# Kernel tuning notes

Hardware: AMD Instinct MI355X
Metric: run time of the kernel (lower is better)

Reference implementation:

```python
import jax, jax.numpy as jnp
import numpy as np

N_LEVELS = 8
N_FEATS = 2
LOG2_T = 19
BASE_RES = 16.0
FINEST_RES = 2048.0
BOX_MIN, BOX_MAX = 0.0, 1.0
B_GROWTH = float(np.exp((np.log(FINEST_RES) - np.log(BASE_RES)) / (N_LEVELS - 1)))  # = 2.0
HASH_MASK = (1 << LOG2_T) - 1
BATCH = 4194304


def setup_inputs() -> dict:
    key = jax.random.key(0)
    kx, kt = jax.random.split(key)
    x = jax.random.uniform(kx, (BATCH, 1), dtype=jnp.float32, minval=BOX_MIN, maxval=BOX_MAX)
    # n_levels separate embedding tables, init uniform in [-1e-4, 1e-4]
    tables = jax.random.uniform(kt, (N_LEVELS, 1 << LOG2_T, N_FEATS), dtype=jnp.float32,
                                minval=-1e-4, maxval=1e-4)
    return {"x": x, "tables": tables}


def reference(x, tables):
    # x: [B, 1] in [BOX_MIN, BOX_MAX]; tables: [L, 2^T, F]
    outs = []
    for i in range(N_LEVELS):
        resolution = jnp.floor(BASE_RES * (B_GROWTH ** i))
        grid_size = (BOX_MAX - BOX_MIN) / resolution
        idx = jnp.floor((x - BOX_MIN) / grid_size)            # [B, 1] cell index (float)
        interval_min = BOX_MIN + idx * grid_size              # [B, 1]
        interval_max = interval_min + grid_size               # [B, 1]
        # two interval vertices: idx and idx+1; 1-D spatial hash = index & (2^T - 1)
        verts = jnp.concatenate([idx, idx + 1.0], axis=-1).astype(jnp.int32)  # [B, 2]
        hashed = jnp.bitwise_and(verts, HASH_MASK)            # [B, 2]
        emb = tables[i][hashed]                               # [B, 2, F] gather
        w = (x - interval_min) / (interval_max - interval_min)  # [B, 1]
        c = emb[:, 0] * (1.0 - w) + emb[:, 1] * w             # [B, F]
        outs.append(c)
    return jnp.concatenate(outs, axis=-1)                     # [B, L*F]
```

## Files before the change

kernel.cpp:

```cpp
#include <hip/hip_runtime.h>


#define NGP_BATCH   4194304
#define NGP_TSIZE   (1 << 19)
#define BLOCK       512
#define PPB         4096
#define KITER       (PPB / (BLOCK/4))
#define NBODY       (KITER / 4)

typedef float f32x4 __attribute__((ext_vector_type(4)));

__global__ __launch_bounds__(BLOCK) void hashenc_kernel(
    const float* __restrict__ x,
    const float* __restrict__ tables,
    float* __restrict__ out)
{
    __shared__ float4 sm4[4080];

    const int tid = threadIdx.x;

#pragma unroll
    for (int l = 0; l < 8; ++l) {
        const int n   = 16 << l;
        const int off = 16 * ((1 << l) - 1);
        const float2* __restrict__ src =
            reinterpret_cast<const float2*>(tables) + (size_t)l * NGP_TSIZE;
        for (int e = tid; e < n; e += BLOCK) {
            const float2 a = src[e];
            const float2 b = src[e + 1];
            sm4[off + e] = make_float4(a.x, a.y, b.x - a.x, b.y - a.y);
        }
    }
    __syncthreads();

    const int q  = tid >> 2;
    const int s  = tid & 3;
    const int l0 = 2 * s;
    const int l1 = 2 * s + 1;
    const float res0 = (float)(16 << l0);
    const float res1 = (float)(16 << l1);
    const int   off0 = 16 * ((1 << l0) - 1);
    const int   off1 = 16 * ((1 << l1) - 1);

    const int P0 = blockIdx.x * PPB;
    f32x4* __restrict__ out4 = reinterpret_cast<f32x4*>(out);

    float xc[4], xn[4];
#pragma unroll
    for (int j = 0; j < 4; ++j)
        xc[j] = x[P0 + q + 128 * j];

#pragma unroll
    for (int m = 0; m < NBODY; ++m) {
        if (m + 1 < NBODY) {
#pragma unroll
            for (int j = 0; j < 4; ++j)
                xn[j] = x[P0 + q + 128 * (4 * (m + 1) + j)];
        }

#pragma unroll
        for (int j = 0; j < 4; ++j) {
            const int   p  = P0 + q + 128 * (4 * m + j);
            const float xv = xc[j];

            const float fx0 = xv * res0;
            const float fi0 = floorf(fx0);
            const float w0  = fx0 - fi0;
            const float4 e0 = sm4[off0 + (int)fi0];

            const float fx1 = xv * res1;
            const float fi1 = floorf(fx1);
            const float w1  = fx1 - fi1;
            const float4 e1 = sm4[off1 + (int)fi1];

            f32x4 r;
            r.x = fmaf(w0, e0.z, e0.x);
            r.y = fmaf(w0, e0.w, e0.y);
            r.z = fmaf(w1, e1.z, e1.x);
            r.w = fmaf(w1, e1.w, e1.y);

            __builtin_nontemporal_store(r, &out4[(size_t)p * 4 + s]);
        }

        if (m + 1 < NBODY) {
#pragma unroll
            for (int j = 0; j < 4; ++j)
                xc[j] = xn[j];
        }
    }
}

extern "C" void kernel_launch(void* const* d_in, const int* in_sizes, int n_in,
                              void* d_out, int out_size, void* d_ws, size_t ws_size,
                              hipStream_t stream) {
    const float* x      = (const float*)d_in[0];
    const float* tables = (const float*)d_in[1];
    float*       out    = (float*)d_out;

    const int grid = NGP_BATCH / PPB;
    hashenc_kernel<<<grid, BLOCK, 0, stream>>>(x, tables, out);
}
```

Baseline: 51.55 us.

## Map one level per thread with 8 threads per point instead of 4

Each thread now handles a single level for a point, with eight threads covering the eight levels, instead of two levels per thread across four threads. Stores shrink from 16-byte to 8-byte vectors, and each thread processes twice as many points per block (KITER doubles). The aim is to spread work differently and possibly reduce shared-memory bank conflicts. The cost is twice as many x loads and loop iterations per thread, plus narrower stores.

```diff
diff --git a/kernel.cpp b/kernel.cpp
--- a/kernel.cpp
+++ b/kernel.cpp
@@ -5,10 +5,10 @@
 #define NGP_TSIZE   (1 << 19)
 #define BLOCK       512
 #define PPB         4096
-#define KITER       (PPB / (BLOCK/4))
+#define KITER       (PPB / (BLOCK/8))
 #define NBODY       (KITER / 4)
 
-typedef float f32x4 __attribute__((ext_vector_type(4)));
+typedef float f32x2 __attribute__((ext_vector_type(2)));
 
 __global__ __launch_bounds__(BLOCK) void hashenc_kernel(
     const float* __restrict__ x,
@@ -33,53 +33,42 @@
     }
     __syncthreads();
 
-    const int q  = tid >> 2;
-    const int s  = tid & 3;
-    const int l0 = 2 * s;
-    const int l1 = 2 * s + 1;
-    const float res0 = (float)(16 << l0);
-    const float res1 = (float)(16 << l1);
-    const int   off0 = 16 * ((1 << l0) - 1);
-    const int   off1 = 16 * ((1 << l1) - 1);
+    const int q = tid >> 3;
+    const int s = tid & 7;
+    const float res = (float)(16 << s);
+    const int   off = 16 * ((1 << s) - 1);
 
     const int P0 = blockIdx.x * PPB;
-    f32x4* __restrict__ out4 = reinterpret_cast<f32x4*>(out);
+    f32x2* __restrict__ out2 = reinterpret_cast<f32x2*>(out);
 
     float xc[4], xn[4];
 #pragma unroll
     for (int j = 0; j < 4; ++j)
-        xc[j] = x[P0 + q + 128 * j];
+        xc[j] = x[P0 + q + 64 * j];
 
 #pragma unroll
     for (int m = 0; m < NBODY; ++m) {
         if (m + 1 < NBODY) {
 #pragma unroll
             for (int j = 0; j < 4; ++j)
-                xn[j] = x[P0 + q + 128 * (4 * (m + 1) + j)];
+                xn[j] = x[P0 + q + 64 * (4 * (m + 1) + j)];
         }
 
 #pragma unroll
         for (int j = 0; j < 4; ++j) {
-            const int   p  = P0 + q + 128 * (4 * m + j);
+            const int   p  = P0 + q + 64 * (4 * m + j);
             const float xv = xc[j];
 
-            const float fx0 = xv * res0;
-            const float fi0 = floorf(fx0);
-            const float w0  = fx0 - fi0;
-            const float4 e0 = sm4[off0 + (int)fi0];
+            const float fx = xv * res;
+            const float fi = floorf(fx);
+            const float w  = fx - fi;
+            const float4 e = sm4[off + (int)fi];
 
-            const float fx1 = xv * res1;
-            const float fi1 = floorf(fx1);
-            const float w1  = fx1 - fi1;
-            const float4 e1 = sm4[off1 + (int)fi1];
+            f32x2 r;
+            r.x = fmaf(w, e.z, e.x);
+            r.y = fmaf(w, e.w, e.y);
 
-            f32x4 r;
-            r.x = fmaf(w0, e0.z, e0.x);
-            r.y = fmaf(w0, e0.w, e0.y);
-            r.z = fmaf(w1, e1.z, e1.x);
-            r.w = fmaf(w1, e1.w, e1.y);
-
-            __builtin_nontemporal_store(r, &out4[(size_t)p * 4 + s]);
+            __builtin_nontemporal_store(r, &out2[(size_t)p * 8 + s]);
         }
 
         if (m + 1 < NBODY) {
```

After: 55.67 us. 8.0% more time.
